# Performance work log

Hardware: AMD Instinct MI355X
Metric: run time of the kernel (lower is better)

## Reference

```python
import jax, jax.numpy as jnp
import numpy as np

NUM_HEADS = 12

def _elu1(x):
    return jax.nn.elu(x) + 1.0

def setup_inputs() -> dict:
    key = jax.random.key(0)
    ks = jax.random.split(key, 7)
    B, Nq, Nk, D = 8, 4096, 1024, 768
    s = 0.02
    return {
        "x_query": jax.random.normal(ks[0], (B, Nq, D), dtype=jnp.float32),
        "x_key_value": jax.random.normal(ks[1], (B, Nk, D), dtype=jnp.float32),
        "Wq": jax.random.normal(ks[2], (D, D), dtype=jnp.float32) * s,
        "Wk": jax.random.normal(ks[3], (D, D), dtype=jnp.float32) * s,
        "Wv": jax.random.normal(ks[4], (D, D), dtype=jnp.float32) * s,
        "Wo": jax.random.normal(ks[5], (D, D), dtype=jnp.float32) * s,
        "bo": jax.random.normal(ks[6], (D,), dtype=jnp.float32) * s,
    }

def reference(x_query, x_key_value, Wq, Wk, Wv, Wo, bo):
    B, Nq, D = x_query.shape
    Nk = x_key_value.shape[1]
    H = NUM_HEADS
    hd = D // H
    # projections (torch Linear: x @ W.T), split heads -> [B, H, N, hd]
    q = (x_query @ Wq.T).reshape(B, Nq, H, hd).transpose(0, 2, 1, 3)
    k = (x_key_value @ Wk.T).reshape(B, Nk, H, hd).transpose(0, 2, 1, 3)
    v = (x_key_value @ Wv.T).reshape(B, Nk, H, hd).transpose(0, 2, 1, 3)
    q = _elu1(q)
    k = _elu1(k)
    # kv: [B,H,hd,hd]; k_sum: [B,H,hd]
    kv = jnp.einsum('bhnd,bhne->bhde', k, v)
    k_sum = k.sum(axis=2)
    z = 1.0 / (jnp.einsum('bhqd,bhd->bhq', q, k_sum) + 1e-6)  # [B,H,Nq]
    attn_out = jnp.einsum('bhqd,bhde->bhqe', q, kv) * z[..., None]
    attn_out = attn_out.transpose(0, 2, 1, 3).reshape(B, Nq, D)
    return attn_out @ Wo.T + bo
```

## Files before the change

kernel.cpp:

```cpp
#include <hip/hip_runtime.h>

typedef _Float16 half8_t __attribute__((ext_vector_type(8)));
typedef _Float16 half4_t __attribute__((ext_vector_type(4)));
typedef float    float4_t __attribute__((ext_vector_type(4)));

#define DIM 768

#define GLOAD16(g, l) __builtin_amdgcn_global_load_lds(                        \
    (const __attribute__((address_space(1))) void*)(g),                        \
    (__attribute__((address_space(3))) void*)(l), 16, 0, 0)

#define MFMA16(a, b, c) __builtin_amdgcn_mfma_f32_16x16x32_f16((a), (b), (c), 0, 0, 0)

__global__ __launch_bounds__(256) void cast_all(
    const float* __restrict__ xq,  const float* __restrict__ xkv,
    const float* __restrict__ Wq,  const float* __restrict__ Wk,
    const float* __restrict__ Wv,  const float* __restrict__ Wo,
    _Float16* __restrict__ dq, _Float16* __restrict__ dkv,
    _Float16* __restrict__ dW )
{
    int i = blockIdx.x * 256 + threadIdx.x;
    const float* s; _Float16* d; int off;
    if (i < 3145728)      { s = xq;  d = dq;  off = i; }
    else if (i < 3932160) { s = xkv; d = dkv; off = i - 3145728; }
    else {
        int j = i - 3932160;
        int w = j / 73728;  off = j - w * 73728;
        s = (w == 0) ? Wq : (w == 1) ? Wk : (w == 2) ? Wv : Wo;
        d = dW + (size_t)w * 589824;
    }
    float4_t f0 = *(const float4_t*)&s[(size_t)off * 8];
    float4_t f1 = *(const float4_t*)&s[(size_t)off * 8 + 4];
    half8_t h;
    #pragma unroll
    for (int e = 0; e < 4; ++e) { h[e] = (_Float16)f0[e]; h[e + 4] = (_Float16)f1[e]; }
    *(half8_t*)&d[(size_t)off * 8] = h;
}

__device__ __forceinline__ void gemm_core(const _Float16* __restrict__ A,
                                          const _Float16* __restrict__ W,
                                          int row0, int col0,
                                          _Float16* lds, float4_t acc[8][4])
{
    const int tid  = threadIdx.x;
    const int wid  = tid >> 6, lane = tid & 63;
    const int wr   = wid >> 2;
    const int wc   = wid & 3;

    const int srow = 2 * wid * 16 + (lane & 15);
    const int sk   = (lane >> 4) * 8;
    const _Float16* As0 = A + (size_t)(row0 + srow) * DIM + sk;
    const _Float16* As1 = As0 + (size_t)16 * DIM;
    const _Float16* Bs0 = W + (size_t)(col0 + srow) * DIM + sk;
    const _Float16* Bs1 = Bs0 + (size_t)16 * DIM;

#define STAGE_A(t, s) do {                                                     \
        GLOAD16(As0 + (t) * 32, &lds[(s) * 16384 + (2*wid    ) * 512]);        \
        GLOAD16(As1 + (t) * 32, &lds[(s) * 16384 + (2*wid + 1) * 512]);        \
    } while (0)
#define STAGE_B(t, s) do {                                                     \
        GLOAD16(Bs0 + (t) * 32, &lds[(s) * 16384 + 8192 + (2*wid    ) * 512]); \
        GLOAD16(Bs1 + (t) * 32, &lds[(s) * 16384 + 8192 + (2*wid + 1) * 512]); \
    } while (0)

    const int ab = (wr * 8) * 512 + lane * 8;
    const int bb = 8192 + (wc * 4) * 512 + lane * 8;

    STAGE_A(0, 0); STAGE_B(0, 0);
    STAGE_A(1, 1); STAGE_B(1, 1);
    asm volatile("s_waitcnt vmcnt(4)" ::: "memory");
    __builtin_amdgcn_s_barrier();

    int s = 0, s2 = 2;
    for (int t = 0; t < 24; ++t) {
        const _Float16* sl = &lds[s * 16384];
        const bool pf = (t < 22);

        half8_t bf[4], af[4];
        #pragma unroll
        for (int ni = 0; ni < 4; ++ni)
            bf[ni] = *(const half8_t*)&sl[bb + ni * 512];
        #pragma unroll
        for (int mi = 0; mi < 4; ++mi)
            af[mi] = *(const half8_t*)&sl[ab + mi * 512];
        if (pf) STAGE_A(t + 2, s2);
        __builtin_amdgcn_s_barrier();
        asm volatile("s_waitcnt lgkmcnt(0)" ::: "memory");
        __builtin_amdgcn_sched_barrier(0);
        __builtin_amdgcn_s_setprio(1);
        #pragma unroll
        for (int mi = 0; mi < 4; ++mi)
            #pragma unroll
            for (int ni = 0; ni < 4; ++ni)
                acc[mi][ni] = MFMA16(af[mi], bf[ni], acc[mi][ni]);
        __builtin_amdgcn_s_setprio(0);
        __builtin_amdgcn_sched_barrier(0);
        __builtin_amdgcn_s_barrier();

        half8_t af1[4];
        #pragma unroll
        for (int mi = 0; mi < 4; ++mi)
            af1[mi] = *(const half8_t*)&sl[ab + (4 + mi) * 512];
        if (pf) STAGE_B(t + 2, s2);
        __builtin_amdgcn_s_barrier();
        asm volatile("s_waitcnt lgkmcnt(0)" ::: "memory");
        __builtin_amdgcn_sched_barrier(0);
        __builtin_amdgcn_s_setprio(1);
        #pragma unroll
        for (int mi = 0; mi < 4; ++mi)
            #pragma unroll
            for (int ni = 0; ni < 4; ++ni)
                acc[4 + mi][ni] = MFMA16(af1[mi], bf[ni], acc[4 + mi][ni]);
        __builtin_amdgcn_s_setprio(0);
        __builtin_amdgcn_sched_barrier(0);

        if (t < 23) {
            if (pf) asm volatile("s_waitcnt vmcnt(4)" ::: "memory");
            else    asm volatile("s_waitcnt vmcnt(0)" ::: "memory");
            __builtin_amdgcn_s_barrier();
        }
        s  = (s  == 2) ? 0 : s  + 1;
        s2 = (s2 == 2) ? 0 : s2 + 1;
    }
#undef STAGE_A
#undef STAGE_B
}

__global__ __launch_bounds__(512) void proj_qkv(
    const _Float16* __restrict__ xq16, const _Float16* __restrict__ xkv16,
    const _Float16* __restrict__ Wq16, const _Float16* __restrict__ Wk16,
    const _Float16* __restrict__ Wv16,
    _Float16* __restrict__ q16, _Float16* __restrict__ k16,
    _Float16* __restrict__ v16)
{
    __shared__ __align__(16) _Float16 lds[3 * 16384];

    const int cpx = gridDim.x >> 3;
    int bid = (blockIdx.x & 7) * cpx + (blockIdx.x >> 3);

    const _Float16 *A, *W; _Float16* O; bool elu;
    int brow, bcol;
    if (bid < 384) {
        A = xq16; W = Wq16; O = q16; elu = true;
        brow = bid / 3; bcol = bid - brow * 3;
    } else {
        int u = bid - 384;
        int mat = u / 96;  u -= mat * 96;
        A = xkv16; W = mat ? Wv16 : Wk16; O = mat ? v16 : k16; elu = !mat;
        brow = u / 3; bcol = u - brow * 3;
    }
    const int row0 = brow * 256, col0 = bcol * 256;

    float4_t acc[8][4] = {};
    gemm_core(A, W, row0, col0, lds, acc);

    const int wid = threadIdx.x >> 6, lane = threadIdx.x & 63;
    const int wr = wid >> 2, wc = wid & 3, lr = lane & 15, lkg = lane >> 4;
    #pragma unroll
    for (int mi = 0; mi < 8; ++mi) {
        #pragma unroll
        for (int ni = 0; ni < 4; ++ni) {
            #pragma unroll
            for (int e = 0; e < 4; ++e) {
                int r = row0 + wr * 128 + mi * 16 + lkg * 4 + e;
                int c = col0 + wc * 64 + ni * 16 + lr;
                float v = acc[mi][ni][e];
                if (elu) v = (v > 0.0f) ? (v + 1.0f) : __expf(v);
                O[(size_t)r * DIM + c] = (_Float16)v;
            }
        }
    }
}

__global__ __launch_bounds__(512) void out_proj(
    const _Float16* __restrict__ a16, const _Float16* __restrict__ Wo16,
    const float* __restrict__ bo, float* __restrict__ out)
{
    __shared__ __align__(16) _Float16 lds[3 * 16384];

    const int cpx = gridDim.x >> 3;
    int bid = (blockIdx.x & 7) * cpx + (blockIdx.x >> 3);
    const int brow = bid / 3, bcol = bid - brow * 3;
    const int row0 = brow * 256, col0 = bcol * 256;

    float4_t acc[8][4] = {};
    gemm_core(a16, Wo16, row0, col0, lds, acc);

    const int wid = threadIdx.x >> 6, lane = threadIdx.x & 63;
    const int wr = wid >> 2, wc = wid & 3, lr = lane & 15, lkg = lane >> 4;
    #pragma unroll
    for (int mi = 0; mi < 8; ++mi) {
        #pragma unroll
        for (int ni = 0; ni < 4; ++ni) {
            #pragma unroll
            for (int e = 0; e < 4; ++e) {
                int r = row0 + wr * 128 + mi * 16 + lkg * 4 + e;
                int c = col0 + wc * 64 + ni * 16 + lr;
                out[(size_t)r * DIM + c] = acc[mi][ni][e] + bo[c];
            }
        }
    }
}

__global__ __launch_bounds__(256) void kv_reduce(const _Float16* __restrict__ k16,
                                                 const _Float16* __restrict__ v16,
                                                 float* __restrict__ kvh,
                                                 float* __restrict__ ksum)
{
    __shared__ __align__(16) _Float16 K[128][64];
    __shared__ __align__(16) _Float16 V[128][64];
    const int chunk = blockIdx.x;
    const int bh    = blockIdx.y;
    const int b = bh / 12, h = bh % 12;
    const int tid = threadIdx.x;

    const size_t base = ((size_t)b * 1024 + (size_t)chunk * 128) * DIM + h * 64;
    #pragma unroll
    for (int j = 0; j < 4; ++j) {
        int idx = j * 256 + tid;
        int r = idx >> 3, c = (idx & 7) * 8;
        *(half8_t*)&K[r][c] = *(const half8_t*)&k16[base + (size_t)r * DIM + c];
        *(half8_t*)&V[r][c] = *(const half8_t*)&v16[base + (size_t)r * DIM + c];
    }
    __syncthreads();

    const int d0 = (tid & 15) * 4;
    const int e0 = (tid >> 4) * 4;
    float acc[4][4] = {};
    #pragma unroll 4
    for (int n = 0; n < 128; ++n) {
        half4_t kd = *(const half4_t*)&K[n][d0];
        half4_t ve = *(const half4_t*)&V[n][e0];
        #pragma unroll
        for (int i = 0; i < 4; ++i)
            #pragma unroll
            for (int j = 0; j < 4; ++j)
                acc[i][j] += (float)ve[i] * (float)kd[j];
    }
    float* kvp = kvh + (size_t)bh * 64 * 64;
    #pragma unroll
    for (int i = 0; i < 4; ++i)
        #pragma unroll
        for (int j = 0; j < 4; ++j)
            atomicAdd(&kvp[(e0 + i) * 64 + d0 + j], acc[i][j]);

    if (tid < 64) {
        float s = 0.0f;
        for (int n = 0; n < 128; ++n) s += (float)K[n][tid];
        atomicAdd(&ksum[bh * 64 + tid], s);
    }
}

__global__ __launch_bounds__(256) void attn_kernel(_Float16* __restrict__ q16,
                                                   const float* __restrict__ kvh,
                                                   const float* __restrict__ ksum)
{
    __shared__ __align__(16) _Float16 Q[128][72];
    __shared__ __align__(16) _Float16 Bv[64][72];
    __shared__ float S[64];
    __shared__ float Z[128];

    const int h    = blockIdx.x;
    const int rb   = blockIdx.y;
    const int row0 = rb * 128;
    const int b    = row0 >> 12;
    const int bh   = b * 12 + h;
    const int tid  = threadIdx.x;

    #pragma unroll
    for (int j = 0; j < 4; ++j) {
        int idx = j * 256 + tid;
        int r = idx >> 3, c = (idx & 7) * 8;
        *(half8_t*)&Q[r][c] =
            *(const half8_t*)&q16[(size_t)(row0 + r) * DIM + h * 64 + c];
    }
    #pragma unroll
    for (int j = 0; j < 4; ++j) {
        int idx = j * 256 + tid;
        int r = idx >> 4, c = (idx & 15) * 4;
        float4_t f = *(const float4_t*)&kvh[((size_t)bh * 64 + r) * 64 + c];
        half4_t hh;
        #pragma unroll
        for (int e = 0; e < 4; ++e) hh[e] = (_Float16)f[e];
        *(half4_t*)&Bv[r][c] = hh;
    }
    if (tid < 64) S[tid] = ksum[bh * 64 + tid];
    __syncthreads();

    if (tid < 128) {
        float dot = 0.0f;
        #pragma unroll 8
        for (int d = 0; d < 64; ++d) dot += (float)Q[tid][d] * S[d];
        Z[tid] = 1.0f / (dot + 1e-6f);
    }
    __syncthreads();

    const int w = tid >> 6, lane = tid & 63;
    const int lr = lane & 15, lkg = lane >> 4;
    float4_t acc[2][4] = {};
    #pragma unroll
    for (int kc = 0; kc < 2; ++kc) {
        half8_t aF[2], bF[4];
        #pragma unroll
        for (int mi = 0; mi < 2; ++mi)
            aF[mi] = *(const half8_t*)&Q[w * 32 + mi * 16 + lr][kc * 32 + lkg * 8];
        #pragma unroll
        for (int ni = 0; ni < 4; ++ni)
            bF[ni] = *(const half8_t*)&Bv[ni * 16 + lr][kc * 32 + lkg * 8];
        #pragma unroll
        for (int mi = 0; mi < 2; ++mi)
            #pragma unroll
            for (int ni = 0; ni < 4; ++ni)
                acc[mi][ni] = MFMA16(aF[mi], bF[ni], acc[mi][ni]);
    }
    #pragma unroll
    for (int mi = 0; mi < 2; ++mi) {
        #pragma unroll
        for (int ni = 0; ni < 4; ++ni) {
            #pragma unroll
            for (int e = 0; e < 4; ++e) {
                int r = w * 32 + mi * 16 + lkg * 4 + e;
                float v = acc[mi][ni][e] * Z[r];
                q16[(size_t)(row0 + r) * DIM + h * 64 + ni * 16 + lr] = (_Float16)v;
            }
        }
    }
}

extern "C" void kernel_launch(void* const* d_in, const int* in_sizes, int n_in,
                              void* d_out, int out_size, void* d_ws, size_t ws_size,
                              hipStream_t stream)
{
    const float* xq  = (const float*)d_in[0];
    const float* xkv = (const float*)d_in[1];
    const float* Wq  = (const float*)d_in[2];
    const float* Wk  = (const float*)d_in[3];
    const float* Wv  = (const float*)d_in[4];
    const float* Wo  = (const float*)d_in[5];
    const float* bo  = (const float*)d_in[6];

    char* ws = (char*)d_ws;
    const size_t SZ_Q16   = (size_t)32768 * 768 * 2;
    const size_t SZ_XKV16 = (size_t)8192 * 768 * 2;
    const size_t SZ_W16   = (size_t)768 * 768 * 2;
    const size_t SZ_KVH   = (size_t)96 * 64 * 64 * 4;
    const size_t SZ_KSUM  = (size_t)96 * 64 * 4;

    _Float16* q16   = (_Float16*)(ws);
    _Float16* xkv16 = (_Float16*)(ws + SZ_Q16);
    _Float16* Wq16  = (_Float16*)(ws + SZ_Q16 + SZ_XKV16);
    _Float16* Wk16  = (_Float16*)(ws + SZ_Q16 + SZ_XKV16 + SZ_W16);
    _Float16* Wv16  = (_Float16*)(ws + SZ_Q16 + SZ_XKV16 + 2 * SZ_W16);
    _Float16* Wo16  = (_Float16*)(ws + SZ_Q16 + SZ_XKV16 + 3 * SZ_W16);
    float*    kvh   = (float*)   (ws + SZ_Q16 + SZ_XKV16 + 4 * SZ_W16);
    float*    ksum  = (float*)   (ws + SZ_Q16 + SZ_XKV16 + 4 * SZ_W16 + SZ_KVH);

    char* ob = (char*)d_out;
    _Float16* xq16 = (_Float16*)(ob);
    _Float16* k16  = (_Float16*)(ob + 50331648);
    _Float16* v16  = (_Float16*)(ob + 50331648 + 12582912);
    float*    out  = (float*)d_out;

    cast_all<<<16512, 256, 0, stream>>>(xq, xkv, Wq, Wk, Wv, Wo,
                                        xq16, xkv16, Wq16);
    hipMemsetAsync(kvh, 0, SZ_KVH + SZ_KSUM, stream);

    proj_qkv<<<576, 512, 0, stream>>>(xq16, xkv16, Wq16, Wk16, Wv16,
                                      q16, k16, v16);

    kv_reduce<<<dim3(8, 96), 256, 0, stream>>>(k16, v16, kvh, ksum);
    attn_kernel<<<dim3(12, 256), 256, 0, stream>>>(q16, kvh, ksum);

    out_proj<<<384, 512, 0, stream>>>(q16, Wo16, bo, out);
}
```

Baseline: 253.5 us.

## Deepen GEMM LDS pipeline to four stages with one barrier per k-step

Moves the shared GEMM core from a 3-buffer, prefetch-distance-2 pipeline with split A/B staging and four barriers per k-step to a 4-buffer ring with prefetch distance 3. All fragments are loaded at once and each k-step issues 32 MFMAs with a single barrier. The goal is to hide more global-load latency and cut synchronisation overhead. In exchange, LDS per block grows from 96KB to 128KB and register pressure rises from holding 8 A fragments at once, which may limit occupancy.

```diff
diff --git a/kernel.cpp b/kernel.cpp
--- a/kernel.cpp
+++ b/kernel.cpp
@@ -54,11 +54,9 @@
     const _Float16* Bs0 = W + (size_t)(col0 + srow) * DIM + sk;
     const _Float16* Bs1 = Bs0 + (size_t)16 * DIM;
 
-#define STAGE_A(t, s) do {                                                     \
+#define STAGE(t, s) do {                                                       \
         GLOAD16(As0 + (t) * 32, &lds[(s) * 16384 + (2*wid    ) * 512]);        \
         GLOAD16(As1 + (t) * 32, &lds[(s) * 16384 + (2*wid + 1) * 512]);        \
-    } while (0)
-#define STAGE_B(t, s) do {                                                     \
         GLOAD16(Bs0 + (t) * 32, &lds[(s) * 16384 + 8192 + (2*wid    ) * 512]); \
         GLOAD16(Bs1 + (t) * 32, &lds[(s) * 16384 + 8192 + (2*wid + 1) * 512]); \
     } while (0)
@@ -66,64 +64,43 @@
     const int ab = (wr * 8) * 512 + lane * 8;
     const int bb = 8192 + (wc * 4) * 512 + lane * 8;
 
-    STAGE_A(0, 0); STAGE_B(0, 0);
-    STAGE_A(1, 1); STAGE_B(1, 1);
-    asm volatile("s_waitcnt vmcnt(4)" ::: "memory");
+    STAGE(0, 0); STAGE(1, 1); STAGE(2, 2);
+    asm volatile("s_waitcnt vmcnt(8)" ::: "memory");
     __builtin_amdgcn_s_barrier();
-
-    int s = 0, s2 = 2;
+    __builtin_amdgcn_sched_barrier(0);
+
     for (int t = 0; t < 24; ++t) {
-        const _Float16* sl = &lds[s * 16384];
-        const bool pf = (t < 22);
-
-        half8_t bf[4], af[4];
+        const _Float16* sl = &lds[(t & 3) * 16384];
+
+        half8_t bf[4], af[8];
         #pragma unroll
         for (int ni = 0; ni < 4; ++ni)
             bf[ni] = *(const half8_t*)&sl[bb + ni * 512];
         #pragma unroll
-        for (int mi = 0; mi < 4; ++mi)
+        for (int mi = 0; mi < 8; ++mi)
             af[mi] = *(const half8_t*)&sl[ab + mi * 512];
-        if (pf) STAGE_A(t + 2, s2);
-        __builtin_amdgcn_s_barrier();
+        if (t < 21) STAGE(t + 3, (t + 3) & 3);
+
         asm volatile("s_waitcnt lgkmcnt(0)" ::: "memory");
         __builtin_amdgcn_sched_barrier(0);
         __builtin_amdgcn_s_setprio(1);
         #pragma unroll
-        for (int mi = 0; mi < 4; ++mi)
+        for (int mi = 0; mi < 8; ++mi)
             #pragma unroll
             for (int ni = 0; ni < 4; ++ni)
                 acc[mi][ni] = MFMA16(af[mi], bf[ni], acc[mi][ni]);
         __builtin_amdgcn_s_setprio(0);
         __builtin_amdgcn_sched_barrier(0);
-        __builtin_amdgcn_s_barrier();
-
-        half8_t af1[4];
-        #pragma unroll
-        for (int mi = 0; mi < 4; ++mi)
-            af1[mi] = *(const half8_t*)&sl[ab + (4 + mi) * 512];
-        if (pf) STAGE_B(t + 2, s2);
-        __builtin_amdgcn_s_barrier();
-        asm volatile("s_waitcnt lgkmcnt(0)" ::: "memory");
-        __builtin_amdgcn_sched_barrier(0);
-        __builtin_amdgcn_s_setprio(1);
-        #pragma unroll
-        for (int mi = 0; mi < 4; ++mi)
-            #pragma unroll
-            for (int ni = 0; ni < 4; ++ni)
-                acc[4 + mi][ni] = MFMA16(af1[mi], bf[ni], acc[4 + mi][ni]);
-        __builtin_amdgcn_s_setprio(0);
-        __builtin_amdgcn_sched_barrier(0);
 
         if (t < 23) {
-            if (pf) asm volatile("s_waitcnt vmcnt(4)" ::: "memory");
-            else    asm volatile("s_waitcnt vmcnt(0)" ::: "memory");
+            if (t < 21)       asm volatile("s_waitcnt vmcnt(8)" ::: "memory");
+            else if (t == 21) asm volatile("s_waitcnt vmcnt(4)" ::: "memory");
+            else              asm volatile("s_waitcnt vmcnt(0)" ::: "memory");
             __builtin_amdgcn_s_barrier();
+            __builtin_amdgcn_sched_barrier(0);
         }
-        s  = (s  == 2) ? 0 : s  + 1;
-        s2 = (s2 == 2) ? 0 : s2 + 1;
-    }
-#undef STAGE_A
-#undef STAGE_B
+    }
+#undef STAGE
 }
 
 __global__ __launch_bounds__(512) void proj_qkv(
@@ -133,7 +110,7 @@
     _Float16* __restrict__ q16, _Float16* __restrict__ k16,
     _Float16* __restrict__ v16)
 {
-    __shared__ __align__(16) _Float16 lds[3 * 16384];
+    __shared__ __align__(16) _Float16 lds[4 * 16384];
 
     const int cpx = gridDim.x >> 3;
     int bid = (blockIdx.x & 7) * cpx + (blockIdx.x >> 3);
@@ -176,7 +153,7 @@
     const _Float16* __restrict__ a16, const _Float16* __restrict__ Wo16,
     const float* __restrict__ bo, float* __restrict__ out)
 {
-    __shared__ __align__(16) _Float16 lds[3 * 16384];
+    __shared__ __align__(16) _Float16 lds[4 * 16384];
 
     const int cpx = gridDim.x >> 3;
     int bid = (blockIdx.x & 7) * cpx + (blockIdx.x >> 3);
```

Result: no change. 255.0 us (+0.6%).
